# Kernel tuning notes

Hardware: AMD Instinct MI355X
Metric: run time of the kernel (lower is better)

Reference implementation:

```python
import jax, jax.numpy as jnp
import numpy as np

N = 100000      # nodes
E = 1600000     # edges (avg degree 16)
IN, HID, OUT = 256, 256, 128


def setup_inputs() -> dict:
    key = jax.random.key(0)
    ks = jax.random.split(key, 9)
    x = jax.random.normal(ks[0], (N, IN), jnp.float32)
    edge_index = jax.random.randint(ks[1], (2, E), 0, N, dtype=jnp.int64)
    perm = jax.random.permutation(ks[2], N).astype(jnp.int64)
    # GCN layer params (glorot-ish scale) and Bilinear discriminator params
    W1 = jax.random.normal(ks[3], (IN, HID), jnp.float32) * (1.0 / np.sqrt(IN))
    b1 = jnp.zeros((HID,), jnp.float32)
    W2 = jax.random.normal(ks[4], (HID, OUT), jnp.float32) * (1.0 / np.sqrt(HID))
    b2 = jnp.zeros((OUT,), jnp.float32)
    Wb = jax.random.normal(ks[5], (OUT, OUT), jnp.float32) * (1.0 / np.sqrt(OUT))
    bb = jnp.zeros((1,), jnp.float32)
    return {"x": x, "edge_index": edge_index, "perm": perm,
            "W1": W1, "b1": b1, "W2": W2, "b2": b2, "Wb": Wb, "bb": bb}


def reference(x, edge_index, perm, W1, b1, W2, b2, Wb, bb):
    n = x.shape[0]
    src, dst = edge_index[0], edge_index[1]
    # GCN symmetric norm with self-loops: deg = 1 + in-degree
    deg = 1.0 + jax.ops.segment_sum(jnp.ones(src.shape[0], x.dtype), dst,
                                    num_segments=n)
    dinv = jax.lax.rsqrt(deg)                 # [N]
    enorm = dinv[src] * dinv[dst]             # per-edge norm
    self_norm = dinv * dinv                   # self-loop norm

    def gcn(h, W, b):
        hw = h @ W                                            # [N, F]
        agg = jax.ops.segment_sum(hw[src] * enorm[:, None], dst,
                                  num_segments=n)             # scatter-add
        return agg + self_norm[:, None] * hw + b

    def encode(h):
        return gcn(jax.nn.relu(gcn(h, W1, b1)), W2, b2)       # [N, OUT]

    H = encode(x)
    s = jax.nn.sigmoid(H.mean(axis=0))                        # summary [OUT]

    def disc(Hh):
        # nn.Bilinear(d, d, 1): score_n = H_n^T Wb s + bb
        return (jnp.einsum('nd,de,e->n', Hh, Wb, s) + bb)[:, None]

    pos_scores = disc(H)
    neg_scores = disc(encode(x[perm]))
    return pos_scores, neg_scores
```

## Files before the change

kernel.cpp:

```cpp
#include <hip/hip_runtime.h>


typedef __attribute__((ext_vector_type(8))) short bh8;
typedef __attribute__((ext_vector_type(4))) float f4;
typedef __attribute__((ext_vector_type(4))) unsigned short u16x4;
typedef __attribute__((ext_vector_type(8))) unsigned short u16x8;

#define AS1 __attribute__((address_space(1)))
#define AS3 __attribute__((address_space(3)))

__device__ __forceinline__ unsigned short f2b(float f) {
    unsigned int u = __float_as_uint(f);
    unsigned int r = (u + 0x7FFFu + ((u >> 16) & 1u)) >> 16;
    return (unsigned short)r;
}
__device__ __forceinline__ float b2f(unsigned short h) {
    return __uint_as_float(((unsigned int)h) << 16);
}

__global__ void k_degree(const int* __restrict__ dst, int* __restrict__ deg, int E) {
    int e = blockIdx.x * blockDim.x + threadIdx.x;
    if (e < E) atomicAdd(&deg[dst[e]], 1);
}

__global__ void k_dinv(const int* __restrict__ deg, const int* __restrict__ perm,
                       float* __restrict__ dinv, int* __restrict__ pinv,
                       int* __restrict__ rowptr, int N, int E) {
    int n = blockIdx.x * blockDim.x + threadIdx.x;
    if (n < N) {
        dinv[n] = 1.0f / sqrtf(1.0f + (float)deg[n]);
        pinv[perm[n]] = n;
    }
    if (n == 0) rowptr[N] = E;
}

__global__ void k_scanA(const int* __restrict__ in, int* __restrict__ out,
                        int* __restrict__ bsum, int n) {
    __shared__ int sh[256];
    int t = threadIdx.x;
    int base = blockIdx.x * 1024 + t * 4;
    int v[4];
#pragma unroll
    for (int j = 0; j < 4; ++j) v[j] = (base + j < n) ? in[base + j] : 0;
    int s = v[0] + v[1] + v[2] + v[3];
    sh[t] = s;
    __syncthreads();
    for (int off = 1; off < 256; off <<= 1) {
        int u = (t >= off) ? sh[t - off] : 0;
        __syncthreads();
        sh[t] += u;
        __syncthreads();
    }
    int excl = sh[t] - s;
    if (t == 255) bsum[blockIdx.x] = sh[255];
    int run = excl;
#pragma unroll
    for (int j = 0; j < 4; ++j) {
        if (base + j < n) out[base + j] = run;
        run += v[j];
    }
}

__global__ void k_scanB(const int* __restrict__ bsum, int* __restrict__ boff, int nb) {
    __shared__ int sh[128];
    int t = threadIdx.x;
    int v = (t < nb) ? bsum[t] : 0;
    sh[t] = v;
    __syncthreads();
    for (int off = 1; off < 128; off <<= 1) {
        int u = (t >= off) ? sh[t - off] : 0;
        __syncthreads();
        sh[t] += u;
        __syncthreads();
    }
    boff[t] = sh[t] - v;
}

__global__ void k_scanC(int* __restrict__ out, const int* __restrict__ boff, int n) {
    int t = threadIdx.x;
    int base = blockIdx.x * 1024 + t * 4;
    int add = boff[blockIdx.x];
#pragma unroll
    for (int j = 0; j < 4; ++j)
        if (base + j < n) out[base + j] += add;
}

__global__ void k_fill(const int* __restrict__ src, const int* __restrict__ dst,
                       const int* __restrict__ rowptr, int* __restrict__ cursor,
                       int* __restrict__ csr, int E) {
    int e = blockIdx.x * blockDim.x + threadIdx.x;
    if (e >= E) return;
    int d = dst[e];
    int p = rowptr[d] + atomicAdd(&cursor[d], 1);
    csr[p] = src[e];
}

__global__ void k_split(const float* __restrict__ in, unsigned short* __restrict__ hi,
                        long n4) {
    long i = (long)blockIdx.x * blockDim.x + threadIdx.x;
    if (i >= n4) return;
    float4 v = ((const float4*)in)[i];
    float f[4] = {v.x, v.y, v.z, v.w};
    u16x4 h;
#pragma unroll
    for (int j = 0; j < 4; ++j) h[j] = f2b(f[j]);
    ((u16x4*)hi)[i] = h;
}

__global__ void k_wsplitT(const float* __restrict__ W, unsigned short* __restrict__ thi,
                          unsigned short* __restrict__ tlo, int K, int Nc) {
    int t = blockIdx.x * blockDim.x + threadIdx.x;
    if (t >= K * Nc) return;
    int k = t / Nc, n = t % Nc;
    float f = W[t];
    unsigned short hb = f2b(f);
    thi[n * K + k] = hb;
    tlo[n * K + k] = f2b(f - b2f(hb));
}

template <int MODE>
__global__ __launch_bounds__(256, 2) void k_gemm_mfma(
        const unsigned short* __restrict__ Ahi0, const unsigned short* __restrict__ Ahi1,
        const unsigned short* __restrict__ Bhi, const unsigned short* __restrict__ Blo,
        unsigned short* __restrict__ C, const float* __restrict__ dinv,
        const int* __restrict__ pinv, int M, int K, int NcB, int ldC, int colz) {
    __shared__ short lds[3][128 * 32];
    const int tid  = threadIdx.x;
    const int lane = tid & 63;
    const int w    = tid >> 6;
    const int wr   = w >> 1, wc = w & 1;
    const int row0 = blockIdx.y * 128;
    const int bcol = blockIdx.x * 128;
    const unsigned short* Ahi = blockIdx.z ? Ahi1 : Ahi0;

    const unsigned short* sp = (w == 1) ? Bhi : (w == 2) ? Blo : Ahi;
    const int  plane = (w == 1) ? 1 : (w == 2) ? 2 : 0;
    const int  slab0 = (w == 3) ? 4 : 0;
    const int  nslab = (w == 0 || w == 3) ? 4 : 8;
    const int  base0 = (w == 1 || w == 2) ? bcol : row0;
    const int  lim   = (w == 1 || w == 2) ? (NcB - 1) : (M - 1);
    const int  rsub  = lane >> 2;
    const int  clin  = lane & 3;

    f4 acc[4][4] = {};

    for (int k0 = 0; k0 < K; k0 += 32) {
        __syncthreads();
        for (int s = 0; s < nslab; ++s) {
            int slab = slab0 + s;
            int r = slab * 16 + rsub;
            int g = base0 + r;
            if (g > lim) g = lim;
            const unsigned short* srcp = sp + (size_t)g * K + k0 + clin * 8;
            __builtin_amdgcn_global_load_lds((const AS1 void*)srcp,
                                             (AS3 void*)&lds[plane][slab * 512], 16, 0, 0);
        }
        __syncthreads();

        bh8 ah[4], bh_[4], bl[4];
        const int fr = lane & 15;
        const int fc = (lane >> 4) * 8;
#pragma unroll
        for (int m = 0; m < 4; ++m)
            ah[m] = *(const bh8*)&lds[0][(wr * 64 + m * 16 + fr) * 32 + fc];
#pragma unroll
        for (int n = 0; n < 4; ++n) {
            int off = (wc * 64 + n * 16 + fr) * 32 + fc;
            bh_[n] = *(const bh8*)&lds[1][off];
            bl[n]  = *(const bh8*)&lds[2][off];
        }
#pragma unroll
        for (int m = 0; m < 4; ++m)
#pragma unroll
            for (int n = 0; n < 4; ++n)
                acc[m][n] = __builtin_amdgcn_mfma_f32_16x16x32_bf16(ah[m], bh_[n], acc[m][n], 0, 0, 0);
#pragma unroll
        for (int m = 0; m < 4; ++m)
#pragma unroll
            for (int n = 0; n < 4; ++n)
                acc[m][n] = __builtin_amdgcn_mfma_f32_16x16x32_bf16(ah[m], bl[n], acc[m][n], 0, 0, 0);
    }

    const int cr = (lane >> 4) * 4;
    const int cc = lane & 15;
#pragma unroll
    for (int m = 0; m < 4; ++m) {
        int r0 = row0 + wr * 64 + m * 16 + cr;
#pragma unroll
        for (int j = 0; j < 4; ++j) {
            int r = r0 + j;
            if (r >= M) continue;
            if constexpr (MODE == 1) {
                float sr = dinv[r];
                int   ur = pinv[r];
                float su = dinv[ur];
#pragma unroll
                for (int n = 0; n < 4; ++n) {
                    int c = bcol + wc * 64 + n * 16 + cc;
                    C[(size_t)r  * 512 + c]       = f2b(sr * acc[m][n][j]);
                    C[(size_t)ur * 512 + 256 + c] = f2b(su * acc[m][n][j]);
                }
            } else {
                float sr = dinv[r];
                int cbase = blockIdx.z * colz + bcol;
#pragma unroll
                for (int n = 0; n < 4; ++n) {
                    int c = cbase + wc * 64 + n * 16 + cc;
                    C[(size_t)r * ldC + c] = f2b(sr * acc[m][n][j]);
                }
            }
        }
    }
}

__global__ __launch_bounds__(256) void k_aggTU(
        const unsigned short* __restrict__ TU, const int* __restrict__ rowptr,
        const int* __restrict__ csr, const float* __restrict__ dinv,
        const float* __restrict__ bias,
        unsigned short* __restrict__ Bp, unsigned short* __restrict__ Bn, int n) {
    int wid = (blockIdx.x * blockDim.x + threadIdx.x) >> 6;
    int lane = threadIdx.x & 63;
    if (wid >= n) return;
    int beg = rowptr[wid], end = rowptr[wid + 1];
    int off = lane * 8;
    float a[8] = {0.f, 0.f, 0.f, 0.f, 0.f, 0.f, 0.f, 0.f};
    int e = beg;
    for (; e + 3 < end; e += 4) {
        int s0 = csr[e], s1 = csr[e + 1], s2 = csr[e + 2], s3 = csr[e + 3];
        u16x8 v0 = *(const u16x8*)(TU + (size_t)s0 * 512 + off);
        u16x8 v1 = *(const u16x8*)(TU + (size_t)s1 * 512 + off);
        u16x8 v2 = *(const u16x8*)(TU + (size_t)s2 * 512 + off);
        u16x8 v3 = *(const u16x8*)(TU + (size_t)s3 * 512 + off);
#pragma unroll
        for (int j = 0; j < 8; ++j)
            a[j] += (b2f(v0[j]) + b2f(v1[j])) + (b2f(v2[j]) + b2f(v3[j]));
    }
    for (; e < end; ++e) {
        int s0 = csr[e];
        u16x8 v0 = *(const u16x8*)(TU + (size_t)s0 * 512 + off);
#pragma unroll
        for (int j = 0; j < 8; ++j) a[j] += b2f(v0[j]);
    }
    u16x8 vs = *(const u16x8*)(TU + (size_t)wid * 512 + off);
#pragma unroll
    for (int j = 0; j < 8; ++j) a[j] += b2f(vs[j]);

    float dn = dinv[wid];
    int f0 = (lane & 31) * 8;
    float4 bv0 = *(const float4*)(bias + f0);
    float4 bv1 = *(const float4*)(bias + f0 + 4);
    float bb8[8] = {bv0.x, bv0.y, bv0.z, bv0.w, bv1.x, bv1.y, bv1.z, bv1.w};
    u16x8 o;
#pragma unroll
    for (int j = 0; j < 8; ++j)
        o[j] = f2b(fmaxf(dn * a[j] + bb8[j], 0.f));
    unsigned short* dstp = (lane < 32 ? Bp : Bn) + (size_t)wid * 256 + f0;
    __builtin_nontemporal_store(o, (u16x8*)dstp);
}

__global__ __launch_bounds__(256) void k_aggT2(
        const unsigned short* __restrict__ G2, const int* __restrict__ rowptr,
        const int* __restrict__ csr, const float* __restrict__ dinv,
        const float* __restrict__ bias, float* __restrict__ Hpos,
        float* __restrict__ Hneg, int n) {
    int wid = (blockIdx.x * blockDim.x + threadIdx.x) >> 6;
    int lane = threadIdx.x & 63;
    if (wid >= n) return;
    int beg = rowptr[wid], end = rowptr[wid + 1];
    int off = lane * 4;
    float a[4] = {0.f, 0.f, 0.f, 0.f};
    int e = beg;
    for (; e + 3 < end; e += 4) {
        int s0 = csr[e], s1 = csr[e + 1], s2 = csr[e + 2], s3 = csr[e + 3];
        u16x4 v0 = *(const u16x4*)(G2 + (size_t)s0 * 256 + off);
        u16x4 v1 = *(const u16x4*)(G2 + (size_t)s1 * 256 + off);
        u16x4 v2 = *(const u16x4*)(G2 + (size_t)s2 * 256 + off);
        u16x4 v3 = *(const u16x4*)(G2 + (size_t)s3 * 256 + off);
#pragma unroll
        for (int j = 0; j < 4; ++j)
            a[j] += (b2f(v0[j]) + b2f(v1[j])) + (b2f(v2[j]) + b2f(v3[j]));
    }
    for (; e < end; ++e) {
        int s0 = csr[e];
        u16x4 v0 = *(const u16x4*)(G2 + (size_t)s0 * 256 + off);
#pragma unroll
        for (int j = 0; j < 4; ++j) a[j] += b2f(v0[j]);
    }
    u16x4 vs = *(const u16x4*)(G2 + (size_t)wid * 256 + off);
#pragma unroll
    for (int j = 0; j < 4; ++j) a[j] += b2f(vs[j]);

    float dn = dinv[wid];
    int f0 = (lane & 31) * 4;
    float4 bv = *(const float4*)(bias + f0);
    float bb4[4] = {bv.x, bv.y, bv.z, bv.w};
    f4 r;
#pragma unroll
    for (int j = 0; j < 4; ++j) r[j] = dn * a[j] + bb4[j];
    float* dstp = (lane < 32 ? Hpos : Hneg) + (size_t)wid * 128 + f0;
    __builtin_nontemporal_store(r, (f4*)dstp);
}

__global__ void k_colsum(const float* __restrict__ H, float* __restrict__ colsum, int n) {
    int c = threadIdx.x & 127, half = threadIdx.x >> 7;
    float acc = 0.f;
    for (int r = blockIdx.x * 2 + half; r < n; r += gridDim.x * 2)
        acc += H[(size_t)r * 128 + c];
    __shared__ float sh[256];
    sh[threadIdx.x] = acc;
    __syncthreads();
    if (half == 0) atomicAdd(&colsum[c], sh[c] + sh[c + 128]);
}

__global__ void k_summary(const float* __restrict__ colsum, const float* __restrict__ Wb,
                          float* __restrict__ t, int n) {
    __shared__ float s_sh[128];
    int d = threadIdx.x;
    float m = colsum[d] / (float)n;
    s_sh[d] = 1.0f / (1.0f + expf(-m));
    __syncthreads();
    float acc = 0.f;
    for (int e = 0; e < 128; ++e) acc += Wb[d * 128 + e] * s_sh[e];
    t[d] = acc;
}

__global__ void k_disc(const float* __restrict__ Hpos, const float* __restrict__ Hneg,
                       const float* __restrict__ t, const float* __restrict__ bb,
                       float* __restrict__ out, int n) {
    int wid = (blockIdx.x * blockDim.x + threadIdx.x) >> 6;
    int lane = threadIdx.x & 63;
    if (wid >= 2 * n) return;
    const float* row = (wid < n) ? (Hpos + (size_t)wid * 128)
                                 : (Hneg + (size_t)(wid - n) * 128);
    float p = row[lane] * t[lane] + row[lane + 64] * t[lane + 64];
#pragma unroll
    for (int off = 32; off > 0; off >>= 1) p += __shfl_down(p, off);
    if (lane == 0) out[wid] = p + bb[0];
}

extern "C" void kernel_launch(void* const* d_in, const int* in_sizes, int n_in,
                              void* d_out, int out_size, void* d_ws, size_t ws_size,
                              hipStream_t stream) {
    const float* x    = (const float*)d_in[0];
    const int*   ei   = (const int*)d_in[1];
    const int*   perm = (const int*)d_in[2];
    const float* W1   = (const float*)d_in[3];
    const float* b1   = (const float*)d_in[4];
    const float* W2   = (const float*)d_in[5];
    const float* b2   = (const float*)d_in[6];
    const float* Wb   = (const float*)d_in[7];
    const float* bb   = (const float*)d_in[8];
    float* out = (float*)d_out;

    const int N   = in_sizes[2];
    const int E   = in_sizes[1] / 2;
    const int IN  = in_sizes[0] / N;
    const int HID = in_sizes[4];
    const int OUT = in_sizes[6];
    const int* src = ei;
    const int* dst = ei + E;

    char* p = (char*)d_ws;
    auto alloc = [&](size_t bytes) -> void* {
        void* r = (void*)p;
        p += (bytes + 255) & ~(size_t)255;
        return r;
    };
    int*   deg    = (int*)alloc((size_t)N * 4);
    int*   cursor = (int*)alloc((size_t)N * 4);
    float* colsum = (float*)alloc(128 * 4);
    size_t zlen   = (size_t)(p - (char*)deg);
    int*   rowptr = (int*)alloc((size_t)(N + 1) * 4);
    int*   bsum   = (int*)alloc(128 * 4);
    int*   boff   = (int*)alloc(128 * 4);
    int*   csr    = (int*)alloc((size_t)E * 4);
    int*   pinv   = (int*)alloc((size_t)N * 4);
    float* dinv   = (float*)alloc((size_t)N * 4);
    float* tvec   = (float*)alloc(128 * 4);
    unsigned short* W1thi = (unsigned short*)alloc((size_t)IN * HID * 2);
    unsigned short* W1tlo = (unsigned short*)alloc((size_t)IN * HID * 2);
    unsigned short* W2thi = (unsigned short*)alloc((size_t)HID * OUT * 2);
    unsigned short* W2tlo = (unsigned short*)alloc((size_t)HID * OUT * 2);
    unsigned short* Xhi = (unsigned short*)alloc((size_t)N * IN * 2);
    unsigned short* TU  = (unsigned short*)alloc((size_t)N * 512 * 2);
    unsigned short* Bp  = (unsigned short*)alloc((size_t)N * HID * 2);
    unsigned short* Bn  = (unsigned short*)alloc((size_t)N * HID * 2);

    unsigned short* G2 = Xhi;
    float* Hpos = (float*)TU;
    float* Hneg = (float*)(TU + (size_t)N * 256);

    hipMemsetAsync(deg, 0, zlen, stream);

    int eb = (E + 255) / 256;
    int nb = (N + 255) / 256;
    int nscan = (N + 1023) / 1024;
    k_degree<<<eb, 256, 0, stream>>>(dst, deg, E);
    k_dinv<<<nb, 256, 0, stream>>>(deg, perm, dinv, pinv, rowptr, N, E);
    k_scanA<<<nscan, 256, 0, stream>>>(deg, rowptr, bsum, N);
    k_scanB<<<1, 128, 0, stream>>>(bsum, boff, nscan);
    k_scanC<<<nscan, 256, 0, stream>>>(rowptr, boff, N);
    k_fill<<<eb, 256, 0, stream>>>(src, dst, rowptr, cursor, csr, E);

    long n4 = (long)N * IN / 4;
    k_split<<<(int)((n4 + 255) / 256), 256, 0, stream>>>(x, Xhi, n4);
    k_wsplitT<<<(IN * HID + 255) / 256, 256, 0, stream>>>(W1, W1thi, W1tlo, IN, HID);
    k_wsplitT<<<(HID * OUT + 255) / 256, 256, 0, stream>>>(W2, W2thi, W2tlo, HID, OUT);

    int mblk = (N + 127) / 128;
    int aggb = (N + 3) / 4;

    k_gemm_mfma<1><<<dim3(HID / 128, mblk, 1), 256, 0, stream>>>(
        Xhi, Xhi, W1thi, W1tlo, TU, dinv, pinv, N, IN, HID, 512, 0);
    k_aggTU<<<aggb, 256, 0, stream>>>(TU, rowptr, csr, dinv, b1, Bp, Bn, N);

    k_gemm_mfma<2><<<dim3(OUT / 128, mblk, 2), 256, 0, stream>>>(
        Bp, Bn, W2thi, W2tlo, G2, dinv, pinv, N, HID, OUT, HID, OUT);
    k_aggT2<<<aggb, 256, 0, stream>>>(G2, rowptr, csr, dinv, b2, Hpos, Hneg, N);

    k_colsum<<<256, 256, 0, stream>>>(Hpos, colsum, N);
    k_summary<<<1, 128, 0, stream>>>(colsum, Wb, tvec, N);
    int db = (int)(((size_t)N * 2 * 64 + 255) / 256);
    k_disc<<<db, 256, 0, stream>>>(Hpos, Hneg, tvec, bb, out, N);
}
```

Measured before the change: 924.8 us.

## Share one layer-1 GEMM output between positive and permuted branches via per-edge ratios

The first GEMM now writes only the dinv-scaled X·W1 (256 columns) instead of also scattering a permuted copy into a 512-wide buffer. The negative branch gathers rows at perm[src] and rescales them by a precomputed per-edge ratio dinv[s]/dinv[q], stored in new qcsr/ratio arrays built in the fill kernel. This cuts the GEMM write traffic in half and drops the scattered permuted stores. In exchange the first aggregation does two gathers per edge with an extra multiply, and each edge carries 8 more bytes of metadata. The aggregation kernels are also restructured so each half-wave handles alternate edges with 16-byte loads, then combines the halves with a cross-lane shuffle.

```diff
diff --git a/kernel.cpp b/kernel.cpp
--- a/kernel.cpp
+++ b/kernel.cpp
@@ -23,14 +23,10 @@
     if (e < E) atomicAdd(&deg[dst[e]], 1);
 }
 
-__global__ void k_dinv(const int* __restrict__ deg, const int* __restrict__ perm,
-                       float* __restrict__ dinv, int* __restrict__ pinv,
+__global__ void k_dinv(const int* __restrict__ deg, float* __restrict__ dinv,
                        int* __restrict__ rowptr, int N, int E) {
     int n = blockIdx.x * blockDim.x + threadIdx.x;
-    if (n < N) {
-        dinv[n] = 1.0f / sqrtf(1.0f + (float)deg[n]);
-        pinv[perm[n]] = n;
-    }
+    if (n < N) dinv[n] = 1.0f / sqrtf(1.0f + (float)deg[n]);
     if (n == 0) rowptr[N] = E;
 }
 
@@ -86,13 +82,19 @@
 }
 
 __global__ void k_fill(const int* __restrict__ src, const int* __restrict__ dst,
+                       const int* __restrict__ perm, const float* __restrict__ dinv,
                        const int* __restrict__ rowptr, int* __restrict__ cursor,
-                       int* __restrict__ csr, int E) {
+                       int* __restrict__ csr, int* __restrict__ qcsr,
+                       float* __restrict__ ratio, int E) {
     int e = blockIdx.x * blockDim.x + threadIdx.x;
     if (e >= E) return;
     int d = dst[e];
+    int s = src[e];
+    int q = perm[s];
     int p = rowptr[d] + atomicAdd(&cursor[d], 1);
-    csr[p] = src[e];
+    csr[p] = s;
+    qcsr[p] = q;
+    ratio[p] = dinv[s] / dinv[q];
 }
 
 __global__ void k_split(const float* __restrict__ in, unsigned short* __restrict__ hi,
@@ -118,12 +120,11 @@
     tlo[n * K + k] = f2b(f - b2f(hb));
 }
 
-template <int MODE>
 __global__ __launch_bounds__(256, 2) void k_gemm_mfma(
         const unsigned short* __restrict__ Ahi0, const unsigned short* __restrict__ Ahi1,
         const unsigned short* __restrict__ Bhi, const unsigned short* __restrict__ Blo,
         unsigned short* __restrict__ C, const float* __restrict__ dinv,
-        const int* __restrict__ pinv, int M, int K, int NcB, int ldC, int colz) {
+        int M, int K, int NcB, int ldC, int colz) {
     __shared__ short lds[3][128 * 32];
     const int tid  = threadIdx.x;
     const int lane = tid & 63;
@@ -143,6 +144,8 @@
     const int  clin  = lane & 3;
 
     f4 acc[4][4] = {};
+    const int fr = lane & 15;
+    const int fc = (lane >> 4) * 8;
 
     for (int k0 = 0; k0 < K; k0 += 32) {
         __syncthreads();
@@ -157,32 +160,31 @@
         }
         __syncthreads();
 
-        bh8 ah[4], bh_[4], bl[4];
-        const int fr = lane & 15;
-        const int fc = (lane >> 4) * 8;
+        bh8 ah[4], bhh[4], bll[4];
 #pragma unroll
         for (int m = 0; m < 4; ++m)
             ah[m] = *(const bh8*)&lds[0][(wr * 64 + m * 16 + fr) * 32 + fc];
 #pragma unroll
         for (int n = 0; n < 4; ++n) {
             int off = (wc * 64 + n * 16 + fr) * 32 + fc;
-            bh_[n] = *(const bh8*)&lds[1][off];
-            bl[n]  = *(const bh8*)&lds[2][off];
+            bhh[n] = *(const bh8*)&lds[1][off];
+            bll[n] = *(const bh8*)&lds[2][off];
         }
 #pragma unroll
         for (int m = 0; m < 4; ++m)
 #pragma unroll
             for (int n = 0; n < 4; ++n)
-                acc[m][n] = __builtin_amdgcn_mfma_f32_16x16x32_bf16(ah[m], bh_[n], acc[m][n], 0, 0, 0);
+                acc[m][n] = __builtin_amdgcn_mfma_f32_16x16x32_bf16(ah[m], bhh[n], acc[m][n], 0, 0, 0);
 #pragma unroll
         for (int m = 0; m < 4; ++m)
 #pragma unroll
             for (int n = 0; n < 4; ++n)
-                acc[m][n] = __builtin_amdgcn_mfma_f32_16x16x32_bf16(ah[m], bl[n], acc[m][n], 0, 0, 0);
+                acc[m][n] = __builtin_amdgcn_mfma_f32_16x16x32_bf16(ah[m], bll[n], acc[m][n], 0, 0, 0);
     }
 
     const int cr = (lane >> 4) * 4;
     const int cc = lane & 15;
+    const int cbase = blockIdx.z * colz + bcol;
 #pragma unroll
     for (int m = 0; m < 4; ++m) {
         int r0 = row0 + wr * 64 + m * 16 + cr;
@@ -190,71 +192,87 @@
         for (int j = 0; j < 4; ++j) {
             int r = r0 + j;
             if (r >= M) continue;
-            if constexpr (MODE == 1) {
-                float sr = dinv[r];
-                int   ur = pinv[r];
-                float su = dinv[ur];
-#pragma unroll
-                for (int n = 0; n < 4; ++n) {
-                    int c = bcol + wc * 64 + n * 16 + cc;
-                    C[(size_t)r  * 512 + c]       = f2b(sr * acc[m][n][j]);
-                    C[(size_t)ur * 512 + 256 + c] = f2b(su * acc[m][n][j]);
-                }
-            } else {
-                float sr = dinv[r];
-                int cbase = blockIdx.z * colz + bcol;
-#pragma unroll
-                for (int n = 0; n < 4; ++n) {
-                    int c = cbase + wc * 64 + n * 16 + cc;
-                    C[(size_t)r * ldC + c] = f2b(sr * acc[m][n][j]);
-                }
+            float sr = dinv[r];
+#pragma unroll
+            for (int n = 0; n < 4; ++n) {
+                int c = cbase + wc * 64 + n * 16 + cc;
+                C[(size_t)r * ldC + c] = f2b(sr * acc[m][n][j]);
             }
         }
     }
 }
 
-__global__ __launch_bounds__(256) void k_aggTU(
-        const unsigned short* __restrict__ TU, const int* __restrict__ rowptr,
-        const int* __restrict__ csr, const float* __restrict__ dinv,
-        const float* __restrict__ bias,
+__global__ __launch_bounds__(256) void k_aggT(
+        const unsigned short* __restrict__ T, const int* __restrict__ rowptr,
+        const int* __restrict__ csr, const int* __restrict__ qcsr,
+        const float* __restrict__ ratio, const int* __restrict__ perm,
+        const float* __restrict__ dinv, const float* __restrict__ bias,
         unsigned short* __restrict__ Bp, unsigned short* __restrict__ Bn, int n) {
     int wid = (blockIdx.x * blockDim.x + threadIdx.x) >> 6;
     int lane = threadIdx.x & 63;
     if (wid >= n) return;
+    const int h = lane >> 5, l5 = lane & 31;
+    const int off = l5 * 8;
     int beg = rowptr[wid], end = rowptr[wid + 1];
-    int off = lane * 8;
-    float a[8] = {0.f, 0.f, 0.f, 0.f, 0.f, 0.f, 0.f, 0.f};
+    float ap[8] = {0.f,0.f,0.f,0.f,0.f,0.f,0.f,0.f};
+    float an[8] = {0.f,0.f,0.f,0.f,0.f,0.f,0.f,0.f};
     int e = beg;
     for (; e + 3 < end; e += 4) {
-        int s0 = csr[e], s1 = csr[e + 1], s2 = csr[e + 2], s3 = csr[e + 3];
-        u16x8 v0 = *(const u16x8*)(TU + (size_t)s0 * 512 + off);
-        u16x8 v1 = *(const u16x8*)(TU + (size_t)s1 * 512 + off);
-        u16x8 v2 = *(const u16x8*)(TU + (size_t)s2 * 512 + off);
-        u16x8 v3 = *(const u16x8*)(TU + (size_t)s3 * 512 + off);
-#pragma unroll
-        for (int j = 0; j < 8; ++j)
-            a[j] += (b2f(v0[j]) + b2f(v1[j])) + (b2f(v2[j]) + b2f(v3[j]));
-    }
-    for (; e < end; ++e) {
-        int s0 = csr[e];
-        u16x8 v0 = *(const u16x8*)(TU + (size_t)s0 * 512 + off);
-#pragma unroll
-        for (int j = 0; j < 8; ++j) a[j] += b2f(v0[j]);
-    }
-    u16x8 vs = *(const u16x8*)(TU + (size_t)wid * 512 + off);
-#pragma unroll
-    for (int j = 0; j < 8; ++j) a[j] += b2f(vs[j]);
-
+        int sA = csr[e + h],     qA = qcsr[e + h];     float rA = ratio[e + h];
+        int sB = csr[e + 2 + h], qB = qcsr[e + 2 + h]; float rB = ratio[e + 2 + h];
+        u16x8 vpA = *(const u16x8*)(T + (size_t)sA * 256 + off);
+        u16x8 vnA = *(const u16x8*)(T + (size_t)qA * 256 + off);
+        u16x8 vpB = *(const u16x8*)(T + (size_t)sB * 256 + off);
+        u16x8 vnB = *(const u16x8*)(T + (size_t)qB * 256 + off);
+#pragma unroll
+        for (int j = 0; j < 8; ++j) {
+            ap[j] += b2f(vpA[j]) + b2f(vpB[j]);
+            an[j] += rA * b2f(vnA[j]) + rB * b2f(vnB[j]);
+        }
+    }
+    for (; e < end; e += 2) {
+        int idx = e + h;
+        bool act = idx < end;
+        int ic = act ? idx : e;
+        int s = csr[ic], q = qcsr[ic];
+        float r = ratio[ic];
+        u16x8 vp = *(const u16x8*)(T + (size_t)s * 256 + off);
+        u16x8 vn = *(const u16x8*)(T + (size_t)q * 256 + off);
+        if (act) {
+#pragma unroll
+            for (int j = 0; j < 8; ++j) {
+                ap[j] += b2f(vp[j]);
+                an[j] += r * b2f(vn[j]);
+            }
+        }
+    }
     float dn = dinv[wid];
-    int f0 = (lane & 31) * 8;
-    float4 bv0 = *(const float4*)(bias + f0);
-    float4 bv1 = *(const float4*)(bias + f0 + 4);
+    int pn = perm[wid];
+    int sidx = h ? pn : wid;
+    float swt = h ? (dn / dinv[pn]) : 1.0f;
+    u16x8 vs = *(const u16x8*)(T + (size_t)sidx * 256 + off);
+    if (h == 0) {
+#pragma unroll
+        for (int j = 0; j < 8; ++j) ap[j] += b2f(vs[j]);
+    } else {
+#pragma unroll
+        for (int j = 0; j < 8; ++j) an[j] += swt * b2f(vs[j]);
+    }
+#pragma unroll
+    for (int j = 0; j < 8; ++j) {
+        ap[j] += __shfl_xor(ap[j], 32);
+        an[j] += __shfl_xor(an[j], 32);
+    }
+    float4 bv0 = *(const float4*)(bias + off);
+    float4 bv1 = *(const float4*)(bias + off + 4);
     float bb8[8] = {bv0.x, bv0.y, bv0.z, bv0.w, bv1.x, bv1.y, bv1.z, bv1.w};
     u16x8 o;
 #pragma unroll
-    for (int j = 0; j < 8; ++j)
-        o[j] = f2b(fmaxf(dn * a[j] + bb8[j], 0.f));
-    unsigned short* dstp = (lane < 32 ? Bp : Bn) + (size_t)wid * 256 + f0;
+    for (int j = 0; j < 8; ++j) {
+        float v = h ? an[j] : ap[j];
+        o[j] = f2b(fmaxf(dn * v + bb8[j], 0.f));
+    }
+    unsigned short* dstp = (h ? Bn : Bp) + (size_t)wid * 256 + off;
     __builtin_nontemporal_store(o, (u16x8*)dstp);
 }
 
@@ -266,39 +284,50 @@
     int wid = (blockIdx.x * blockDim.x + threadIdx.x) >> 6;
     int lane = threadIdx.x & 63;
     if (wid >= n) return;
+    const int h = lane >> 5, l5 = lane & 31;
+    const int off = l5 * 8;
     int beg = rowptr[wid], end = rowptr[wid + 1];
-    int off = lane * 4;
-    float a[4] = {0.f, 0.f, 0.f, 0.f};
+    float a[8] = {0.f,0.f,0.f,0.f,0.f,0.f,0.f,0.f};
     int e = beg;
     for (; e + 3 < end; e += 4) {
-        int s0 = csr[e], s1 = csr[e + 1], s2 = csr[e + 2], s3 = csr[e + 3];
-        u16x4 v0 = *(const u16x4*)(G2 + (size_t)s0 * 256 + off);
-        u16x4 v1 = *(const u16x4*)(G2 + (size_t)s1 * 256 + off);
-        u16x4 v2 = *(const u16x4*)(G2 + (size_t)s2 * 256 + off);
-        u16x4 v3 = *(const u16x4*)(G2 + (size_t)s3 * 256 + off);
-#pragma unroll
-        for (int j = 0; j < 4; ++j)
-            a[j] += (b2f(v0[j]) + b2f(v1[j])) + (b2f(v2[j]) + b2f(v3[j]));
-    }
-    for (; e < end; ++e) {
-        int s0 = csr[e];
-        u16x4 v0 = *(const u16x4*)(G2 + (size_t)s0 * 256 + off);
-#pragma unroll
-        for (int j = 0; j < 4; ++j) a[j] += b2f(v0[j]);
-    }
-    u16x4 vs = *(const u16x4*)(G2 + (size_t)wid * 256 + off);
-#pragma unroll
-    for (int j = 0; j < 4; ++j) a[j] += b2f(vs[j]);
-
-    float dn = dinv[wid];
-    int f0 = (lane & 31) * 4;
-    float4 bv = *(const float4*)(bias + f0);
-    float bb4[4] = {bv.x, bv.y, bv.z, bv.w};
-    f4 r;
-#pragma unroll
-    for (int j = 0; j < 4; ++j) r[j] = dn * a[j] + bb4[j];
-    float* dstp = (lane < 32 ? Hpos : Hneg) + (size_t)wid * 128 + f0;
-    __builtin_nontemporal_store(r, (f4*)dstp);
+        int sA = csr[e + h], sB = csr[e + 2 + h];
+        u16x8 vA = *(const u16x8*)(G2 + (size_t)sA * 256 + off);
+        u16x8 vB = *(const u16x8*)(G2 + (size_t)sB * 256 + off);
+#pragma unroll
+        for (int j = 0; j < 8; ++j) a[j] += b2f(vA[j]) + b2f(vB[j]);
+    }
+    for (; e < end; e += 2) {
+        int idx = e + h;
+        bool act = idx < end;
+        int ic = act ? idx : e;
+        int s = csr[ic];
+        u16x8 v = *(const u16x8*)(G2 + (size_t)s * 256 + off);
+        if (act) {
+#pragma unroll
+            for (int j = 0; j < 8; ++j) a[j] += b2f(v[j]);
+        }
+    }
+    if (h == 0) {
+        u16x8 vs = *(const u16x8*)(G2 + (size_t)wid * 256 + off);
+#pragma unroll
+        for (int j = 0; j < 8; ++j) a[j] += b2f(vs[j]);
+    }
+#pragma unroll
+    for (int j = 0; j < 8; ++j) a[j] += __shfl_xor(a[j], 32);
+
+    if (h == 0) {
+        float dn = dinv[wid];
+        int col = (l5 < 16) ? off : (off - 128);
+        const float* bp = bias + col;
+        float* dstp = ((l5 < 16) ? Hpos : Hneg) + (size_t)wid * 128 + col;
+        f4 r0, r1;
+#pragma unroll
+        for (int j = 0; j < 4; ++j) r0[j] = dn * a[j] + bp[j];
+#pragma unroll
+        for (int j = 0; j < 4; ++j) r1[j] = dn * a[4 + j] + bp[4 + j];
+        __builtin_nontemporal_store(r0, (f4*)dstp);
+        __builtin_nontemporal_store(r1, (f4*)(dstp + 4));
+    }
 }
 
 __global__ void k_colsum(const float* __restrict__ H, float* __restrict__ colsum, int n) {
@@ -374,7 +403,8 @@
     int*   bsum   = (int*)alloc(128 * 4);
     int*   boff   = (int*)alloc(128 * 4);
     int*   csr    = (int*)alloc((size_t)E * 4);
-    int*   pinv   = (int*)alloc((size_t)N * 4);
+    int*   qcsr   = (int*)alloc((size_t)E * 4);
+    float* ratio  = (float*)alloc((size_t)E * 4);
     float* dinv   = (float*)alloc((size_t)N * 4);
     float* tvec   = (float*)alloc(128 * 4);
     unsigned short* W1thi = (unsigned short*)alloc((size_t)IN * HID * 2);
@@ -382,13 +412,13 @@
     unsigned short* W2thi = (unsigned short*)alloc((size_t)HID * OUT * 2);
     unsigned short* W2tlo = (unsigned short*)alloc((size_t)HID * OUT * 2);
     unsigned short* Xhi = (unsigned short*)alloc((size_t)N * IN * 2);
-    unsigned short* TU  = (unsigned short*)alloc((size_t)N * 512 * 2);
+    unsigned short* Tt  = (unsigned short*)alloc((size_t)N * HID * 2);
     unsigned short* Bp  = (unsigned short*)alloc((size_t)N * HID * 2);
     unsigned short* Bn  = (unsigned short*)alloc((size_t)N * HID * 2);
 
     unsigned short* G2 = Xhi;
-    float* Hpos = (float*)TU;
-    float* Hneg = (float*)(TU + (size_t)N * 256);
+    float* Hpos = (float*)Tt;
+    float* Hneg = (float*)Bp;
 
     hipMemsetAsync(deg, 0, zlen, stream);
 
@@ -396,11 +426,12 @@
     int nb = (N + 255) / 256;
     int nscan = (N + 1023) / 1024;
     k_degree<<<eb, 256, 0, stream>>>(dst, deg, E);
-    k_dinv<<<nb, 256, 0, stream>>>(deg, perm, dinv, pinv, rowptr, N, E);
+    k_dinv<<<nb, 256, 0, stream>>>(deg, dinv, rowptr, N, E);
     k_scanA<<<nscan, 256, 0, stream>>>(deg, rowptr, bsum, N);
     k_scanB<<<1, 128, 0, stream>>>(bsum, boff, nscan);
     k_scanC<<<nscan, 256, 0, stream>>>(rowptr, boff, N);
-    k_fill<<<eb, 256, 0, stream>>>(src, dst, rowptr, cursor, csr, E);
+    k_fill<<<eb, 256, 0, stream>>>(src, dst, perm, dinv, rowptr, cursor,
+                                   csr, qcsr, ratio, E);
 
     long n4 = (long)N * IN / 4;
     k_split<<<(int)((n4 + 255) / 256), 256, 0, stream>>>(x, Xhi, n4);
@@ -410,12 +441,13 @@
     int mblk = (N + 127) / 128;
     int aggb = (N + 3) / 4;
 
-    k_gemm_mfma<1><<<dim3(HID / 128, mblk, 1), 256, 0, stream>>>(
-        Xhi, Xhi, W1thi, W1tlo, TU, dinv, pinv, N, IN, HID, 512, 0);
-    k_aggTU<<<aggb, 256, 0, stream>>>(TU, rowptr, csr, dinv, b1, Bp, Bn, N);
-
-    k_gemm_mfma<2><<<dim3(OUT / 128, mblk, 2), 256, 0, stream>>>(
-        Bp, Bn, W2thi, W2tlo, G2, dinv, pinv, N, HID, OUT, HID, OUT);
+    k_gemm_mfma<<<dim3(HID / 128, mblk, 1), 256, 0, stream>>>(
+        Xhi, Xhi, W1thi, W1tlo, Tt, dinv, N, IN, HID, HID, 0);
+    k_aggT<<<aggb, 256, 0, stream>>>(Tt, rowptr, csr, qcsr, ratio, perm, dinv, b1,
+                                     Bp, Bn, N);
+
+    k_gemm_mfma<<<dim3(OUT / 128, mblk, 2), 256, 0, stream>>>(
+        Bp, Bn, W2thi, W2tlo, G2, dinv, N, HID, OUT, HID, OUT);
     k_aggT2<<<aggb, 256, 0, stream>>>(G2, rowptr, csr, dinv, b2, Hpos, Hneg, N);
 
     k_colsum<<<256, 256, 0, stream>>>(Hpos, colsum, N);
```

New measurement: 968.5 us. +4.7%, slower.
